# Kernel tuning notes

Hardware: AMD Instinct MI355X
Metric: run time of the kernel (lower is better)

## Reference

```python
import jax, jax.numpy as jnp
import numpy as np

DIM = 768
HEADS = 12
HEAD_DIM = DIM // HEADS
SCALE = HEAD_DIM ** -0.5
EPS = 1e-6


def setup_inputs() -> dict:
    key = jax.random.key(0)
    ks = jax.random.split(key, 10)
    B, Nq, Nk, C = 4, 4096, 4096, DIM
    std = C ** -0.5
    return {
        "x_q": jax.random.normal(ks[0], (B, Nq, C), jnp.float32),
        "x_kv": jax.random.normal(ks[1], (B, Nk, C), jnp.float32),
        "Wq": jax.random.normal(ks[2], (C, C), jnp.float32) * std,
        "bq": jnp.zeros((C,), jnp.float32),
        "Wk": jax.random.normal(ks[3], (C, C), jnp.float32) * std,
        "bk": jnp.zeros((C,), jnp.float32),
        "Wv": jax.random.normal(ks[4], (C, C), jnp.float32) * std,
        "bv": jnp.zeros((C,), jnp.float32),
        "Wp": jax.random.normal(ks[5], (C, C), jnp.float32) * std,
        "bp": jnp.zeros((C,), jnp.float32),
    }


def _phi(x):
    # ELU(alpha=1) + 1 positive feature map
    return jax.nn.elu(x) + 1.0


def reference(x_q, x_kv, Wq, bq, Wk, bk, Wv, bv, Wp, bp):
    B, Nq, C = x_q.shape
    Nk = x_kv.shape[1]
    h, d = HEADS, HEAD_DIM
    # projections (torch Linear: x @ W.T + b)
    q = x_q @ Wq.T + bq   # [B,Nq,C]
    k = x_kv @ Wk.T + bk  # [B,Nk,C]
    v = x_kv @ Wv.T + bv  # [B,Nk,C]
    # split heads -> [B,h,N,d]
    q = q.reshape(B, Nq, h, d).transpose(0, 2, 1, 3) * SCALE
    k = k.reshape(B, Nk, h, d).transpose(0, 2, 1, 3)
    v = v.reshape(B, Nk, h, d).transpose(0, 2, 1, 3)
    q_phi = _phi(q)
    k_phi = _phi(k)
    # KV state [B,h,d,d] and normalizer sum [B,h,d]
    kv = jnp.einsum('bhnd,bhne->bhde', k_phi, v)
    k_sum = k_phi.sum(axis=2)
    out = jnp.einsum('bhnd,bhde->bhne', q_phi, kv)
    z = jnp.einsum('bhnd,bhd->bhn', q_phi, k_sum)[..., None] + EPS
    out = out / z
    out = out.transpose(0, 2, 1, 3).reshape(B, Nq, C)
    return out @ Wp.T + bp
```

## Files before the change

### kernel.cpp

```cpp
#include <hip/hip_runtime.h>
#include <hip/hip_bf16.h>
#include <cstdint>
#include <cstddef>

#define HD_B   4
#define SEQ    4096
#define CDIM   768
#define HEADS  12
#define HDIM   64
#define MROWS  (HD_B * SEQ)
#define QSCALE 0.125f
#define EPSV   1e-6f

typedef __attribute__((ext_vector_type(8))) short  short8v;
typedef __attribute__((ext_vector_type(4))) float  f32x4;

__device__ __forceinline__ unsigned short f2b(float f) {
    unsigned int u = __float_as_uint(f);
    u += 0x7FFFu + ((u >> 16) & 1u);
    return (unsigned short)(u >> 16);
}
__device__ __forceinline__ float b2f(unsigned short b) {
    return __uint_as_float(((unsigned int)b) << 16);
}
__device__ __forceinline__ float phi_f(float x) {
    return x > 0.f ? x + 1.f : __expf(x);
}

#define GLOAD_LDS16(g, l)                                             \
    __builtin_amdgcn_global_load_lds(                                 \
        (__attribute__((address_space(1))) void*)(void*)(g),          \
        (__attribute__((address_space(3))) void*)(l), 16, 0, 0)

#define VMW12() asm volatile("s_waitcnt vmcnt(12)" ::: "memory")
#define VMW8()  asm volatile("s_waitcnt vmcnt(8)"  ::: "memory")
#define VMW4()  asm volatile("s_waitcnt vmcnt(4)"  ::: "memory")
#define VMW0()  asm volatile("s_waitcnt vmcnt(0)"  ::: "memory")
#define LGW()   asm volatile("s_waitcnt lgkmcnt(0)" ::: "memory")
#define SB()    do { __builtin_amdgcn_sched_barrier(0);               \
                     __builtin_amdgcn_s_barrier();                    \
                     __builtin_amdgcn_sched_barrier(0); } while (0)

__global__ void wcvt_all(const float* __restrict__ wq, const float* __restrict__ wk,
                         const float* __restrict__ wv, const float* __restrict__ wp,
                         unsigned short* __restrict__ dst) {
    const int y = blockIdx.y;
    const float* src = (y == 0) ? wq : (y == 1) ? wk : (y == 2) ? wv : wp;
    const int i = blockIdx.x * 256 + threadIdx.x;
    float4 v = reinterpret_cast<const float4*>(src)[i];
    ushort4 o;
    o.x = f2b(v.x); o.y = f2b(v.y); o.z = f2b(v.z); o.w = f2b(v.w);
    reinterpret_cast<ushort4*>(dst + (size_t)y * (CDIM * CDIM))[i] = o;
}

__global__ __launch_bounds__(256) void gemm_q(
    const float* __restrict__ A32,
    const unsigned short* __restrict__ Bp,
    const float* __restrict__ bias,
    unsigned short* __restrict__ outp)
{
    constexpr int K = CDIM;
    __shared__ __align__(16) char smem[32768];
    char* As = smem;
    char* Bs = smem + 16384;

    const int tid  = threadIdx.x;
    const int lane = tid & 63;
    const int w    = tid >> 6;
    const int wr   = w >> 1, wc = w & 1;
    const int brow = blockIdx.x * 128;
    const int bcol = blockIdx.y * 128;

    const int r8  = lane >> 3;
    const int c8e = ((lane & 7) ^ r8) << 3;
    const int ar  = lane >> 4;
    const int ac  = (lane & 15) << 2;
    const int fr  = lane & 15;
    const int hi4 = lane >> 4;

    f32x4 acc[4][4];
#pragma unroll
    for (int i = 0; i < 4; ++i)
#pragma unroll
        for (int j = 0; j < 4; ++j)
            acc[i][j] = (f32x4){0.f, 0.f, 0.f, 0.f};

    for (int k0 = 0; k0 < K; k0 += 64) {
#pragma unroll
        for (int g = 0; g < 4; ++g) {
            const unsigned short* src =
                Bp + (size_t)(bcol + w * 32 + g * 8 + r8) * K + k0 + c8e;
            GLOAD_LDS16(src, Bs + (w * 32 + g * 8) * 128);
        }
#pragma unroll
        for (int j = 0; j < 8; ++j) {
            const int row = w * 32 + j * 4 + ar;
            float4 f = *(const float4*)(A32 + (size_t)(brow + row) * K + k0 + ac);
            unsigned int p0, p1;
            asm("v_cvt_pk_bf16_f32 %0, %1, %2" : "=v"(p0) : "v"(f.x), "v"(f.y));
            asm("v_cvt_pk_bf16_f32 %0, %1, %2" : "=v"(p1) : "v"(f.z), "v"(f.w));
            uint2 pk; pk.x = p0; pk.y = p1;
            *(uint2*)(As + row * 128 + ((ac << 1) ^ ((row & 7) << 4))) = pk;
        }
        __syncthreads();

        short8v a[4][2], b[4][2];
#pragma unroll
        for (int i = 0; i < 4; ++i) {
            const int row = wr * 64 + i * 16 + fr;
#pragma unroll
            for (int ks = 0; ks < 2; ++ks)
                a[i][ks] = *(const short8v*)(As + row * 128 +
                              ((((ks << 2) + hi4) ^ (row & 7)) << 4));
        }
#pragma unroll
        for (int j = 0; j < 4; ++j) {
            const int row = wc * 64 + j * 16 + fr;
#pragma unroll
            for (int ks = 0; ks < 2; ++ks)
                b[j][ks] = *(const short8v*)(Bs + row * 128 +
                              ((((ks << 2) + hi4) ^ (row & 7)) << 4));
        }
#pragma unroll
        for (int i = 0; i < 4; ++i)
#pragma unroll
            for (int j = 0; j < 4; ++j) {
                acc[i][j] = __builtin_amdgcn_mfma_f32_16x16x32_bf16(a[i][0], b[j][0], acc[i][j], 0, 0, 0);
                acc[i][j] = __builtin_amdgcn_mfma_f32_16x16x32_bf16(a[i][1], b[j][1], acc[i][j], 0, 0, 0);
            }
        __syncthreads();
    }

    float* ep = (float*)(void*)smem + w * (16 * 68);
    const int rr = lane >> 2;
    const int cb = (lane & 3) * 4;
    float4 bb[4];
#pragma unroll
    for (int q = 0; q < 4; ++q)
        bb[q] = *(const float4*)&bias[bcol + wc * 64 + q * 16 + cb];
#pragma unroll
    for (int i = 0; i < 4; ++i) {
#pragma unroll
        for (int j = 0; j < 4; ++j)
#pragma unroll
            for (int r = 0; r < 4; ++r)
                ep[(hi4 * 4 + r) * 68 + j * 16 + fr] = acc[i][j][r];
#pragma unroll
        for (int q = 0; q < 4; ++q) {
            const int cc = q * 16 + cb;
            f32x4 v = *(const f32x4*)&ep[rr * 68 + cc];
            const int rg = brow + wr * 64 + i * 16 + rr;
            const int cg = bcol + wc * 64 + cc;
            const float4 bq = bb[q];
            ushort4 ov;
            ov.x = f2b(phi_f((v[0] + bq.x) * QSCALE));
            ov.y = f2b(phi_f((v[1] + bq.y) * QSCALE));
            ov.z = f2b(phi_f((v[2] + bq.z) * QSCALE));
            ov.w = f2b(phi_f((v[3] + bq.w) * QSCALE));
            *(ushort4*)(outp + (size_t)rg * 768 + cg) = ov;
        }
    }
}

template <int KIND>
__global__ __launch_bounds__(256, 3) void gemm_p2(
    const float* __restrict__ A32,
    const unsigned short* __restrict__ Abf,
    const unsigned short* __restrict__ Bp,
    const float* __restrict__ b0, const float* __restrict__ b1,
    unsigned short* __restrict__ out_k, unsigned short* __restrict__ out_v,
    float* __restrict__ out_f)
{
    constexpr int K  = CDIM;
    constexpr int NC = (KIND == 0) ? 12 : 6;
    constexpr int T  = NC * 128;
    constexpr int NT = K / 64;

    __shared__ __align__(16) char smem[49152];
    char* As = smem;

    const int tid  = threadIdx.x;
    const int lane = tid & 63;
    const int w    = tid >> 6;
    const int wr   = w >> 1, wc = w & 1;

    const int bid  = blockIdx.x;
    const int s    = (bid & 7) * (T >> 3) + (bid >> 3);
    const int colp = s % NC;
    const int rowp = s / NC;
    const int brow = rowp * 128;
    const int bcol = colp * 128;

    const int r8  = lane >> 3;
    const int c8e = ((lane & 7) ^ r8) << 3;
    const int ar  = lane >> 4;
    const int ac  = (lane & 15) << 2;
    const int fr  = lane & 15;
    const int hi4 = lane >> 4;

    f32x4 acc[4][4];
#pragma unroll
    for (int i = 0; i < 4; ++i)
#pragma unroll
        for (int j = 0; j < 4; ++j)
            acc[i][j] = (f32x4){0.f, 0.f, 0.f, 0.f};

    auto stageB = [&](int buf, int kt) {
        char* dst = smem + 16384 + buf * 16384;
#pragma unroll
        for (int g = 0; g < 4; ++g) {
            const unsigned short* src =
                Bp + (size_t)(bcol + w * 32 + g * 8 + r8) * K + kt * 64 + c8e;
            GLOAD_LDS16(src, dst + (w * 32 + g * 8) * 128);
        }
    };

    float4 fA[8];
    int4   rAb[4];
    auto aload = [&](int kt) {
        if (KIND == 0) {
#pragma unroll
            for (int j = 0; j < 8; ++j)
                fA[j] = *(const float4*)(A32 + (size_t)(brow + w * 32 + j * 4 + ar) * K
                                         + kt * 64 + ac);
        } else {
#pragma unroll
            for (int g = 0; g < 4; ++g)
                rAb[g] = *(const int4*)(Abf + (size_t)(brow + w * 32 + g * 8 + r8) * K
                                        + kt * 64 + ((lane & 7) << 3));
        }
    };
    auto awrite = [&]() {
        if (KIND == 0) {
#pragma unroll
            for (int j = 0; j < 8; ++j) {
                const int row = w * 32 + j * 4 + ar;
                unsigned int p0, p1;
                asm("v_cvt_pk_bf16_f32 %0, %1, %2" : "=v"(p0) : "v"(fA[j].x), "v"(fA[j].y));
                asm("v_cvt_pk_bf16_f32 %0, %1, %2" : "=v"(p1) : "v"(fA[j].z), "v"(fA[j].w));
                uint2 pk; pk.x = p0; pk.y = p1;
                *(uint2*)(As + row * 128 + ((ac << 1) ^ ((row & 7) << 4))) = pk;
            }
        } else {
#pragma unroll
            for (int g = 0; g < 4; ++g) {
                const int row = w * 32 + g * 8 + r8;
                *(int4*)(As + row * 128 + (((lane & 7) ^ r8) << 4)) = rAb[g];
            }
        }
    };
    auto compute = [&](int bbuf) {
        const char* Bb = smem + 16384 + bbuf * 16384;
        short8v a[4][2];
#pragma unroll
        for (int i = 0; i < 4; ++i) {
            const int row = wr * 64 + i * 16 + fr;
#pragma unroll
            for (int ks = 0; ks < 2; ++ks)
                a[i][ks] = *(const short8v*)(As + row * 128 +
                              ((((ks << 2) + hi4) ^ (row & 7)) << 4));
        }
#pragma unroll
        for (int j = 0; j < 4; ++j) {
            const int row = wc * 64 + j * 16 + fr;
            short8v bb0 = *(const short8v*)(Bb + row * 128 + ((hi4 ^ (row & 7)) << 4));
            short8v bb1 = *(const short8v*)(Bb + row * 128 + (((4 + hi4) ^ (row & 7)) << 4));
#pragma unroll
            for (int i = 0; i < 4; ++i) {
                acc[i][j] = __builtin_amdgcn_mfma_f32_16x16x32_bf16(a[i][0], bb0, acc[i][j], 0, 0, 0);
                acc[i][j] = __builtin_amdgcn_mfma_f32_16x16x32_bf16(a[i][1], bb1, acc[i][j], 0, 0, 0);
            }
        }
    };

    aload(0);
    stageB(0, 0);
    VMW4();
    awrite();
    aload(1);
    stageB(1, 1);
    LGW();
    SB();

    for (int t = 0; t < NT; ++t) {
        const int c = t & 1;
        if (t == NT - 1) { VMW0(); }
        else if (KIND == 0) { VMW12(); }
        else { VMW8(); }
        SB();
        compute(c);
        SB();
        if (t < NT - 1) {
            VMW4();
            awrite();
            if (t < NT - 2) { aload(t + 2); stageB(c, t + 2); }
            LGW();
        }
    }

    float* ep = (float*)(void*)smem + w * (16 * 68);
    const int rr = lane >> 2;
    const int cb = (lane & 3) * 4;
    const bool isV = (KIND == 0) && (colp >= 6);
    const float* bptr = (KIND == 1) ? b0 : (isV ? (b1 + (bcol - 768)) : (b0 + bcol));
    const int colbase = ((KIND == 0 && isV) ? bcol - 768 : bcol) + wc * 64;
    unsigned short* o16 = isV ? out_v : out_k;

    float4 bb[4];
#pragma unroll
    for (int q = 0; q < 4; ++q)
        bb[q] = (KIND == 1)
            ? *(const float4*)&bptr[bcol + wc * 64 + q * 16 + cb]
            : *(const float4*)&bptr[wc * 64 + q * 16 + cb];

#pragma unroll
    for (int i = 0; i < 4; ++i) {
#pragma unroll
        for (int j = 0; j < 4; ++j)
#pragma unroll
            for (int r = 0; r < 4; ++r)
                ep[(hi4 * 4 + r) * 68 + j * 16 + fr] = acc[i][j][r];
#pragma unroll
        for (int q = 0; q < 4; ++q) {
            const int cc = q * 16 + cb;
            f32x4 v = *(const f32x4*)&ep[rr * 68 + cc];
            const int rg = brow + wr * 64 + i * 16 + rr;
            const float4 bq = bb[q];
            if (KIND == 1) {
                float4 ov;
                ov.x = v[0] + bq.x; ov.y = v[1] + bq.y;
                ov.z = v[2] + bq.z; ov.w = v[3] + bq.w;
                *(float4*)(out_f + (size_t)rg * 768 + (bcol + wc * 64 + cc)) = ov;
            } else {
                ushort4 ov;
                if (!isV) {
                    ov.x = f2b(phi_f(v[0] + bq.x));
                    ov.y = f2b(phi_f(v[1] + bq.y));
                    ov.z = f2b(phi_f(v[2] + bq.z));
                    ov.w = f2b(phi_f(v[3] + bq.w));
                } else {
                    ov.x = f2b(v[0] + bq.x);
                    ov.y = f2b(v[1] + bq.y);
                    ov.z = f2b(v[2] + bq.z);
                    ov.w = f2b(v[3] + bq.w);
                }
                *(ushort4*)(o16 + (size_t)rg * 768 + (colbase + cc)) = ov;
            }
        }
    }
}

#define KVCH   128
#define KVITER 2
#define NCHUNK 16

__global__ __launch_bounds__(256) void kv_part(
    const unsigned short* __restrict__ kphi,
    const unsigned short* __restrict__ vmat,
    float* __restrict__ part)
{
    const int bh = blockIdx.y;
    const int b  = bh / HEADS, h = bh % HEADS;
    const int c  = blockIdx.x;
    __shared__ float Kl[KVCH][HDIM];
    __shared__ float Vl[KVCH][HDIM];
    const int t  = threadIdx.x;
    const int i  = t >> 2;
    const int jb = t & 3;

    float acc[16];
#pragma unroll
    for (int jj = 0; jj < 16; ++jj) acc[jj] = 0.f;
    float ksum = 0.f;

    for (int it = 0; it < KVITER; ++it) {
        const size_t rbase = (size_t)b * SEQ + (size_t)c * (KVCH * KVITER) + it * KVCH;
        __syncthreads();
        for (int l = 0; l < KVCH / 32; ++l) {
            int row = l * 32 + (t >> 3);
            int col = (t & 7) << 3;
            const size_t g = (rbase + row) * CDIM + h * HDIM + col;
            int4 kk = *(const int4*)(kphi + g);
            int4 vv = *(const int4*)(vmat + g);
            const unsigned short* kp = (const unsigned short*)&kk;
            const unsigned short* vp = (const unsigned short*)&vv;
#pragma unroll
            for (int q = 0; q < 8; ++q) {
                Kl[row][col + q] = b2f(kp[q]);
                Vl[row][col + q] = b2f(vp[q]);
            }
        }
        __syncthreads();
        for (int n = 0; n < KVCH; ++n) {
            float kf = Kl[n][i];
            const float4* vr = (const float4*)&Vl[n][jb * 16];
            float4 v0 = vr[0], v1 = vr[1], v2 = vr[2], v3 = vr[3];
            acc[0]  += kf * v0.x; acc[1]  += kf * v0.y; acc[2]  += kf * v0.z; acc[3]  += kf * v0.w;
            acc[4]  += kf * v1.x; acc[5]  += kf * v1.y; acc[6]  += kf * v1.z; acc[7]  += kf * v1.w;
            acc[8]  += kf * v2.x; acc[9]  += kf * v2.y; acc[10] += kf * v2.z; acc[11] += kf * v2.w;
            acc[12] += kf * v3.x; acc[13] += kf * v3.y; acc[14] += kf * v3.z; acc[15] += kf * v3.w;
            ksum += kf;
        }
    }
    float* op = part + ((size_t)c * 48 + bh) * 4160;
#pragma unroll
    for (int jj = 0; jj < 16; ++jj) op[i * 64 + jb * 16 + jj] = acc[jj];
    if (jb == 0) op[4096 + i] = ksum;
}

__global__ void kv_finalize(const float* __restrict__ part, float* __restrict__ kv) {
    int idx = blockIdx.x * 256 + threadIdx.x;
    if (idx >= 48 * 4160) return;
    float s = 0.f;
    for (int c = 0; c < NCHUNK; ++c) s += part[(size_t)c * 48 * 4160 + idx];
    kv[idx] = s;
}

__global__ __launch_bounds__(256) void attn_apply(
    const unsigned short* __restrict__ qphi,
    const float* __restrict__ kv,
    unsigned short* __restrict__ attn)
{
    const int h  = blockIdx.y;
    const int m0 = blockIdx.x * 64;
    const int b  = m0 >> 12;
    const int bh = b * HEADS + h;
    __shared__ float kvs[HDIM][HDIM];
    __shared__ float ksums[HDIM];
    __shared__ unsigned short ql[64][HDIM];
    const int t = threadIdx.x;
    const float* kvp = kv + (size_t)bh * 4160;
#pragma unroll
    for (int it = 0; it < 4; ++it) {
        int e = it * 1024 + t * 4;
        *(float4*)&kvs[e >> 6][e & 63] = *(const float4*)&kvp[e];
    }
    if (t < 64) ksums[t] = kvp[4096 + t];
#pragma unroll
    for (int it = 0; it < 2; ++it) {
        int row = it * 32 + (t >> 3);
        int col = (t & 7) << 3;
        *(int4*)&ql[row][col] =
            *(const int4*)(qphi + (size_t)(m0 + row) * CDIM + h * HDIM + col);
    }
    __syncthreads();

    const int r  = t >> 2;
    const int jb = t & 3;
    float acc[16];
#pragma unroll
    for (int jj = 0; jj < 16; ++jj) acc[jj] = 0.f;
    float z = 0.f;
    for (int q8 = 0; q8 < 8; ++q8) {
        short8v qv = *(const short8v*)&ql[r][q8 * 8];
#pragma unroll
        for (int dd = 0; dd < 8; ++dd) {
            float qd = b2f((unsigned short)qv[dd]);
            int d = q8 * 8 + dd;
            const float4* kr = (const float4*)&kvs[d][jb * 16];
            float4 k0 = kr[0], k1 = kr[1], k2 = kr[2], k3 = kr[3];
            acc[0]  += qd * k0.x; acc[1]  += qd * k0.y; acc[2]  += qd * k0.z; acc[3]  += qd * k0.w;
            acc[4]  += qd * k1.x; acc[5]  += qd * k1.y; acc[6]  += qd * k1.z; acc[7]  += qd * k1.w;
            acc[8]  += qd * k2.x; acc[9]  += qd * k2.y; acc[10] += qd * k2.z; acc[11] += qd * k2.w;
            acc[12] += qd * k3.x; acc[13] += qd * k3.y; acc[14] += qd * k3.z; acc[15] += qd * k3.w;
            z += qd * ksums[d];
        }
    }
    const float inv = 1.f / (z + EPSV);
    unsigned short* op = attn + (size_t)(m0 + r) * CDIM + h * HDIM + jb * 16;
#pragma unroll
    for (int jj = 0; jj < 16; ++jj) op[jj] = f2b(acc[jj] * inv);
}

extern "C" void kernel_launch(void* const* d_in, const int* in_sizes, int n_in,
                              void* d_out, int out_size, void* d_ws, size_t ws_size,
                              hipStream_t stream)
{
    const float* x_q  = (const float*)d_in[0];
    const float* x_kv = (const float*)d_in[1];
    const float* Wq   = (const float*)d_in[2];
    const float* bq   = (const float*)d_in[3];
    const float* Wk   = (const float*)d_in[4];
    const float* bk   = (const float*)d_in[5];
    const float* Wv   = (const float*)d_in[6];
    const float* bv   = (const float*)d_in[7];
    const float* Wp   = (const float*)d_in[8];
    const float* bp   = (const float*)d_in[9];
    float* out = (float*)d_out;

    char* ws = (char*)d_ws;
    size_t off = 0;
    auto alloc = [&](size_t bytes) -> char* {
        char* p = ws + off;
        off += (bytes + 255) & ~(size_t)255;
        return p;
    };
    const size_t xelems = (size_t)MROWS * CDIM;
    const size_t welems = (size_t)CDIM * CDIM;

    unsigned short* w16    = (unsigned short*)alloc(4 * welems * 2);
    unsigned short* wkv16  = w16 + welems;
    unsigned short* wp16   = w16 + 3 * welems;
    unsigned short* qphi   = (unsigned short*)alloc(xelems * 2);
    unsigned short* kphi   = (unsigned short*)alloc(xelems * 2);
    unsigned short* v16    = (unsigned short*)alloc(xelems * 2);
    unsigned short* attn16 = (unsigned short*)alloc(xelems * 2);
    float* part = (float*)alloc((size_t)NCHUNK * 48 * 4160 * 4);
    float* kvf  = (float*)alloc((size_t)48 * 4160 * 4);

    wcvt_all<<<dim3(576, 4), 256, 0, stream>>>(Wq, Wk, Wv, Wp, w16);

    gemm_q<<<dim3(128, 6), 256, 0, stream>>>(x_q, w16, bq, qphi);

    gemm_p2<0><<<1536, 256, 0, stream>>>(
        x_kv, nullptr, wkv16, bk, bv, kphi, v16, nullptr);

    kv_part<<<dim3(NCHUNK, 48), 256, 0, stream>>>(kphi, v16, part);
    kv_finalize<<<(48 * 4160 + 255) / 256, 256, 0, stream>>>(part, kvf);
    attn_apply<<<dim3(MROWS / 64, HEADS), 256, 0, stream>>>(qphi, kvf, attn16);

    gemm_p2<1><<<768, 256, 0, stream>>>(
        nullptr, attn16, wp16, bp, nullptr, nullptr, nullptr, out);
}
```

Before: 242.2 us.

## Swap Q and output GEMM kernels, add MFMA priority, shrink KV LDS

The Q projection now runs on the double-buffered, tile-swizzled pipelined GEMM body shared with the KV projection. The output projection moves to the simpler single-buffered kernel, which now loads both A and B directly to LDS. s_setprio is raised around the MFMA sections. kv_part keeps K in bf16 in LDS, uses vectorized V stores and requests 3 blocks per CU. Together these aim to improve overlap and occupancy, but the output GEMM may lose the pipelining it had before.

```diff
diff --git a/kernel.cpp b/kernel.cpp
--- a/kernel.cpp
+++ b/kernel.cpp
@@ -33,7 +33,6 @@
         (__attribute__((address_space(3))) void*)(l), 16, 0, 0)
 
 #define VMW12() asm volatile("s_waitcnt vmcnt(12)" ::: "memory")
-#define VMW8()  asm volatile("s_waitcnt vmcnt(8)"  ::: "memory")
 #define VMW4()  asm volatile("s_waitcnt vmcnt(4)"  ::: "memory")
 #define VMW0()  asm volatile("s_waitcnt vmcnt(0)"  ::: "memory")
 #define LGW()   asm volatile("s_waitcnt lgkmcnt(0)" ::: "memory")
@@ -53,23 +52,31 @@
     reinterpret_cast<ushort4*>(dst + (size_t)y * (CDIM * CDIM))[i] = o;
 }
 
-__global__ __launch_bounds__(256) void gemm_q(
+template <int EPI, int NC>
+__device__ __forceinline__ void proj_body(
     const float* __restrict__ A32,
     const unsigned short* __restrict__ Bp,
-    const float* __restrict__ bias,
-    unsigned short* __restrict__ outp)
-{
-    constexpr int K = CDIM;
-    __shared__ __align__(16) char smem[32768];
+    const float* __restrict__ b0, const float* __restrict__ b1,
+    unsigned short* __restrict__ o0, unsigned short* __restrict__ o1)
+{
+    constexpr int K  = CDIM;
+    constexpr int T  = NC * 128;
+    constexpr int NT = K / 64;
+
+    __shared__ __align__(16) char smem[49152];
     char* As = smem;
-    char* Bs = smem + 16384;
 
     const int tid  = threadIdx.x;
     const int lane = tid & 63;
     const int w    = tid >> 6;
     const int wr   = w >> 1, wc = w & 1;
-    const int brow = blockIdx.x * 128;
-    const int bcol = blockIdx.y * 128;
+
+    const int bid  = blockIdx.x;
+    const int s    = (bid & 7) * (T >> 3) + (bid >> 3);
+    const int colp = s % NC;
+    const int rowp = s / NC;
+    const int brow = rowp * 128;
+    const int bcol = colp * 128;
 
     const int r8  = lane >> 3;
     const int c8e = ((lane & 7) ^ r8) << 3;
@@ -85,126 +92,6 @@
         for (int j = 0; j < 4; ++j)
             acc[i][j] = (f32x4){0.f, 0.f, 0.f, 0.f};
 
-    for (int k0 = 0; k0 < K; k0 += 64) {
-#pragma unroll
-        for (int g = 0; g < 4; ++g) {
-            const unsigned short* src =
-                Bp + (size_t)(bcol + w * 32 + g * 8 + r8) * K + k0 + c8e;
-            GLOAD_LDS16(src, Bs + (w * 32 + g * 8) * 128);
-        }
-#pragma unroll
-        for (int j = 0; j < 8; ++j) {
-            const int row = w * 32 + j * 4 + ar;
-            float4 f = *(const float4*)(A32 + (size_t)(brow + row) * K + k0 + ac);
-            unsigned int p0, p1;
-            asm("v_cvt_pk_bf16_f32 %0, %1, %2" : "=v"(p0) : "v"(f.x), "v"(f.y));
-            asm("v_cvt_pk_bf16_f32 %0, %1, %2" : "=v"(p1) : "v"(f.z), "v"(f.w));
-            uint2 pk; pk.x = p0; pk.y = p1;
-            *(uint2*)(As + row * 128 + ((ac << 1) ^ ((row & 7) << 4))) = pk;
-        }
-        __syncthreads();
-
-        short8v a[4][2], b[4][2];
-#pragma unroll
-        for (int i = 0; i < 4; ++i) {
-            const int row = wr * 64 + i * 16 + fr;
-#pragma unroll
-            for (int ks = 0; ks < 2; ++ks)
-                a[i][ks] = *(const short8v*)(As + row * 128 +
-                              ((((ks << 2) + hi4) ^ (row & 7)) << 4));
-        }
-#pragma unroll
-        for (int j = 0; j < 4; ++j) {
-            const int row = wc * 64 + j * 16 + fr;
-#pragma unroll
-            for (int ks = 0; ks < 2; ++ks)
-                b[j][ks] = *(const short8v*)(Bs + row * 128 +
-                              ((((ks << 2) + hi4) ^ (row & 7)) << 4));
-        }
-#pragma unroll
-        for (int i = 0; i < 4; ++i)
-#pragma unroll
-            for (int j = 0; j < 4; ++j) {
-                acc[i][j] = __builtin_amdgcn_mfma_f32_16x16x32_bf16(a[i][0], b[j][0], acc[i][j], 0, 0, 0);
-                acc[i][j] = __builtin_amdgcn_mfma_f32_16x16x32_bf16(a[i][1], b[j][1], acc[i][j], 0, 0, 0);
-            }
-        __syncthreads();
-    }
-
-    float* ep = (float*)(void*)smem + w * (16 * 68);
-    const int rr = lane >> 2;
-    const int cb = (lane & 3) * 4;
-    float4 bb[4];
-#pragma unroll
-    for (int q = 0; q < 4; ++q)
-        bb[q] = *(const float4*)&bias[bcol + wc * 64 + q * 16 + cb];
-#pragma unroll
-    for (int i = 0; i < 4; ++i) {
-#pragma unroll
-        for (int j = 0; j < 4; ++j)
-#pragma unroll
-            for (int r = 0; r < 4; ++r)
-                ep[(hi4 * 4 + r) * 68 + j * 16 + fr] = acc[i][j][r];
-#pragma unroll
-        for (int q = 0; q < 4; ++q) {
-            const int cc = q * 16 + cb;
-            f32x4 v = *(const f32x4*)&ep[rr * 68 + cc];
-            const int rg = brow + wr * 64 + i * 16 + rr;
-            const int cg = bcol + wc * 64 + cc;
-            const float4 bq = bb[q];
-            ushort4 ov;
-            ov.x = f2b(phi_f((v[0] + bq.x) * QSCALE));
-            ov.y = f2b(phi_f((v[1] + bq.y) * QSCALE));
-            ov.z = f2b(phi_f((v[2] + bq.z) * QSCALE));
-            ov.w = f2b(phi_f((v[3] + bq.w) * QSCALE));
-            *(ushort4*)(outp + (size_t)rg * 768 + cg) = ov;
-        }
-    }
-}
-
-template <int KIND>
-__global__ __launch_bounds__(256, 3) void gemm_p2(
-    const float* __restrict__ A32,
-    const unsigned short* __restrict__ Abf,
-    const unsigned short* __restrict__ Bp,
-    const float* __restrict__ b0, const float* __restrict__ b1,
-    unsigned short* __restrict__ out_k, unsigned short* __restrict__ out_v,
-    float* __restrict__ out_f)
-{
-    constexpr int K  = CDIM;
-    constexpr int NC = (KIND == 0) ? 12 : 6;
-    constexpr int T  = NC * 128;
-    constexpr int NT = K / 64;
-
-    __shared__ __align__(16) char smem[49152];
-    char* As = smem;
-
-    const int tid  = threadIdx.x;
-    const int lane = tid & 63;
-    const int w    = tid >> 6;
-    const int wr   = w >> 1, wc = w & 1;
-
-    const int bid  = blockIdx.x;
-    const int s    = (bid & 7) * (T >> 3) + (bid >> 3);
-    const int colp = s % NC;
-    const int rowp = s / NC;
-    const int brow = rowp * 128;
-    const int bcol = colp * 128;
-
-    const int r8  = lane >> 3;
-    const int c8e = ((lane & 7) ^ r8) << 3;
-    const int ar  = lane >> 4;
-    const int ac  = (lane & 15) << 2;
-    const int fr  = lane & 15;
-    const int hi4 = lane >> 4;
-
-    f32x4 acc[4][4];
-#pragma unroll
-    for (int i = 0; i < 4; ++i)
-#pragma unroll
-        for (int j = 0; j < 4; ++j)
-            acc[i][j] = (f32x4){0.f, 0.f, 0.f, 0.f};
-
     auto stageB = [&](int buf, int kt) {
         char* dst = smem + 16384 + buf * 16384;
 #pragma unroll
@@ -216,37 +103,21 @@
     };
 
     float4 fA[8];
-    int4   rAb[4];
     auto aload = [&](int kt) {
-        if (KIND == 0) {
-#pragma unroll
-            for (int j = 0; j < 8; ++j)
-                fA[j] = *(const float4*)(A32 + (size_t)(brow + w * 32 + j * 4 + ar) * K
-                                         + kt * 64 + ac);
-        } else {
-#pragma unroll
-            for (int g = 0; g < 4; ++g)
-                rAb[g] = *(const int4*)(Abf + (size_t)(brow + w * 32 + g * 8 + r8) * K
-                                        + kt * 64 + ((lane & 7) << 3));
-        }
+#pragma unroll
+        for (int j = 0; j < 8; ++j)
+            fA[j] = *(const float4*)(A32 + (size_t)(brow + w * 32 + j * 4 + ar) * K
+                                     + kt * 64 + ac);
     };
     auto awrite = [&]() {
-        if (KIND == 0) {
-#pragma unroll
-            for (int j = 0; j < 8; ++j) {
-                const int row = w * 32 + j * 4 + ar;
-                unsigned int p0, p1;
-                asm("v_cvt_pk_bf16_f32 %0, %1, %2" : "=v"(p0) : "v"(fA[j].x), "v"(fA[j].y));
-                asm("v_cvt_pk_bf16_f32 %0, %1, %2" : "=v"(p1) : "v"(fA[j].z), "v"(fA[j].w));
-                uint2 pk; pk.x = p0; pk.y = p1;
-                *(uint2*)(As + row * 128 + ((ac << 1) ^ ((row & 7) << 4))) = pk;
-            }
-        } else {
-#pragma unroll
-            for (int g = 0; g < 4; ++g) {
-                const int row = w * 32 + g * 8 + r8;
-                *(int4*)(As + row * 128 + (((lane & 7) ^ r8) << 4)) = rAb[g];
-            }
+#pragma unroll
+        for (int j = 0; j < 8; ++j) {
+            const int row = w * 32 + j * 4 + ar;
+            unsigned int p0, p1;
+            asm("v_cvt_pk_bf16_f32 %0, %1, %2" : "=v"(p0) : "v"(fA[j].x), "v"(fA[j].y));
+            asm("v_cvt_pk_bf16_f32 %0, %1, %2" : "=v"(p1) : "v"(fA[j].z), "v"(fA[j].w));
+            uint2 pk; pk.x = p0; pk.y = p1;
+            *(uint2*)(As + row * 128 + ((ac << 1) ^ ((row & 7) << 4))) = pk;
         }
     };
     auto compute = [&](int bbuf) {
@@ -260,6 +131,7 @@
                 a[i][ks] = *(const short8v*)(As + row * 128 +
                               ((((ks << 2) + hi4) ^ (row & 7)) << 4));
         }
+        __builtin_amdgcn_s_setprio(1);
 #pragma unroll
         for (int j = 0; j < 4; ++j) {
             const int row = wc * 64 + j * 16 + fr;
@@ -271,6 +143,7 @@
                 acc[i][j] = __builtin_amdgcn_mfma_f32_16x16x32_bf16(a[i][1], bb1, acc[i][j], 0, 0, 0);
             }
         }
+        __builtin_amdgcn_s_setprio(0);
     };
 
     aload(0);
@@ -284,9 +157,7 @@
 
     for (int t = 0; t < NT; ++t) {
         const int c = t & 1;
-        if (t == NT - 1) { VMW0(); }
-        else if (KIND == 0) { VMW12(); }
-        else { VMW8(); }
+        if (t == NT - 1) { VMW0(); } else { VMW12(); }
         SB();
         compute(c);
         SB();
@@ -301,17 +172,16 @@
     float* ep = (float*)(void*)smem + w * (16 * 68);
     const int rr = lane >> 2;
     const int cb = (lane & 3) * 4;
-    const bool isV = (KIND == 0) && (colp >= 6);
-    const float* bptr = (KIND == 1) ? b0 : (isV ? (b1 + (bcol - 768)) : (b0 + bcol));
-    const int colbase = ((KIND == 0 && isV) ? bcol - 768 : bcol) + wc * 64;
-    unsigned short* o16 = isV ? out_v : out_k;
+    const bool isV = (EPI == 1) && (colp >= 6);
+    const float* bptr = (EPI == 0) ? (b0 + bcol)
+                        : (isV ? (b1 + (bcol - 768)) : (b0 + bcol));
+    const int colbase = ((EPI == 1 && isV) ? bcol - 768 : bcol) + wc * 64;
+    unsigned short* o16 = (EPI == 1 && isV) ? o1 : o0;
 
     float4 bb[4];
 #pragma unroll
     for (int q = 0; q < 4; ++q)
-        bb[q] = (KIND == 1)
-            ? *(const float4*)&bptr[bcol + wc * 64 + q * 16 + cb]
-            : *(const float4*)&bptr[wc * 64 + q * 16 + cb];
+        bb[q] = *(const float4*)&bptr[wc * 64 + q * 16 + cb];
 
 #pragma unroll
     for (int i = 0; i < 4; ++i) {
@@ -326,26 +196,139 @@
             f32x4 v = *(const f32x4*)&ep[rr * 68 + cc];
             const int rg = brow + wr * 64 + i * 16 + rr;
             const float4 bq = bb[q];
-            if (KIND == 1) {
-                float4 ov;
-                ov.x = v[0] + bq.x; ov.y = v[1] + bq.y;
-                ov.z = v[2] + bq.z; ov.w = v[3] + bq.w;
-                *(float4*)(out_f + (size_t)rg * 768 + (bcol + wc * 64 + cc)) = ov;
+            ushort4 ov;
+            if (EPI == 0) {
+                ov.x = f2b(phi_f((v[0] + bq.x) * QSCALE));
+                ov.y = f2b(phi_f((v[1] + bq.y) * QSCALE));
+                ov.z = f2b(phi_f((v[2] + bq.z) * QSCALE));
+                ov.w = f2b(phi_f((v[3] + bq.w) * QSCALE));
+            } else if (!isV) {
+                ov.x = f2b(phi_f(v[0] + bq.x));
+                ov.y = f2b(phi_f(v[1] + bq.y));
+                ov.z = f2b(phi_f(v[2] + bq.z));
+                ov.w = f2b(phi_f(v[3] + bq.w));
             } else {
-                ushort4 ov;
-                if (!isV) {
-                    ov.x = f2b(phi_f(v[0] + bq.x));
-                    ov.y = f2b(phi_f(v[1] + bq.y));
-                    ov.z = f2b(phi_f(v[2] + bq.z));
-                    ov.w = f2b(phi_f(v[3] + bq.w));
-                } else {
-                    ov.x = f2b(v[0] + bq.x);
-                    ov.y = f2b(v[1] + bq.y);
-                    ov.z = f2b(v[2] + bq.z);
-                    ov.w = f2b(v[3] + bq.w);
-                }
-                *(ushort4*)(o16 + (size_t)rg * 768 + (colbase + cc)) = ov;
+                ov.x = f2b(v[0] + bq.x);
+                ov.y = f2b(v[1] + bq.y);
+                ov.z = f2b(v[2] + bq.z);
+                ov.w = f2b(v[3] + bq.w);
             }
+            *(ushort4*)(o16 + (size_t)rg * 768 + (colbase + cc)) = ov;
+        }
+    }
+}
+
+__global__ __launch_bounds__(256, 3) void g_q(
+    const float* __restrict__ xq, const unsigned short* __restrict__ wq,
+    const float* __restrict__ bq, unsigned short* __restrict__ qphi)
+{
+    proj_body<0, 6>(xq, wq, bq, nullptr, qphi, nullptr);
+}
+
+__global__ __launch_bounds__(256, 3) void g_kv(
+    const float* __restrict__ xkv, const unsigned short* __restrict__ wkv,
+    const float* __restrict__ bk, const float* __restrict__ bv,
+    unsigned short* __restrict__ kphi, unsigned short* __restrict__ v16)
+{
+    proj_body<1, 12>(xkv, wkv, bk, bv, kphi, v16);
+}
+
+__global__ __launch_bounds__(256) void g_out(
+    const unsigned short* __restrict__ A16,
+    const unsigned short* __restrict__ Bp,
+    const float* __restrict__ bias,
+    float* __restrict__ outp)
+{
+    constexpr int K = CDIM;
+    __shared__ __align__(16) char smem[32768];
+    char* As = smem;
+    char* Bs = smem + 16384;
+
+    const int tid  = threadIdx.x;
+    const int lane = tid & 63;
+    const int w    = tid >> 6;
+    const int wr   = w >> 1, wc = w & 1;
+    const int brow = blockIdx.x * 128;
+    const int bcol = blockIdx.y * 128;
+
+    const int r8  = lane >> 3;
+    const int c8e = ((lane & 7) ^ r8) << 3;
+    const int fr  = lane & 15;
+    const int hi4 = lane >> 4;
+
+    f32x4 acc[4][4];
+#pragma unroll
+    for (int i = 0; i < 4; ++i)
+#pragma unroll
+        for (int j = 0; j < 4; ++j)
+            acc[i][j] = (f32x4){0.f, 0.f, 0.f, 0.f};
+
+    for (int k0 = 0; k0 < K; k0 += 64) {
+#pragma unroll
+        for (int g = 0; g < 4; ++g) {
+            const unsigned short* srcA =
+                A16 + (size_t)(brow + w * 32 + g * 8 + r8) * K + k0 + c8e;
+            GLOAD_LDS16(srcA, As + (w * 32 + g * 8) * 128);
+            const unsigned short* srcB =
+                Bp + (size_t)(bcol + w * 32 + g * 8 + r8) * K + k0 + c8e;
+            GLOAD_LDS16(srcB, Bs + (w * 32 + g * 8) * 128);
+        }
+        __syncthreads();
+
+        short8v a[4][2], b[4][2];
+#pragma unroll
+        for (int i = 0; i < 4; ++i) {
+            const int row = wr * 64 + i * 16 + fr;
+#pragma unroll
+            for (int ks = 0; ks < 2; ++ks)
+                a[i][ks] = *(const short8v*)(As + row * 128 +
+                              ((((ks << 2) + hi4) ^ (row & 7)) << 4));
+        }
+#pragma unroll
+        for (int j = 0; j < 4; ++j) {
+            const int row = wc * 64 + j * 16 + fr;
+#pragma unroll
+            for (int ks = 0; ks < 2; ++ks)
+                b[j][ks] = *(const short8v*)(Bs + row * 128 +
+                              ((((ks << 2) + hi4) ^ (row & 7)) << 4));
+        }
+        __builtin_amdgcn_s_setprio(1);
+#pragma unroll
+        for (int i = 0; i < 4; ++i)
+#pragma unroll
+            for (int j = 0; j < 4; ++j) {
+                acc[i][j] = __builtin_amdgcn_mfma_f32_16x16x32_bf16(a[i][0], b[j][0], acc[i][j], 0, 0, 0);
+                acc[i][j] = __builtin_amdgcn_mfma_f32_16x16x32_bf16(a[i][1], b[j][1], acc[i][j], 0, 0, 0);
+            }
+        __builtin_amdgcn_s_setprio(0);
+        __syncthreads();
+    }
+
+    float* ep = (float*)(void*)smem + w * (16 * 68);
+    const int rr = lane >> 2;
+    const int cb = (lane & 3) * 4;
+    float4 bb[4];
+#pragma unroll
+    for (int q = 0; q < 4; ++q)
+        bb[q] = *(const float4*)&bias[bcol + wc * 64 + q * 16 + cb];
+#pragma unroll
+    for (int i = 0; i < 4; ++i) {
+#pragma unroll
+        for (int j = 0; j < 4; ++j)
+#pragma unroll
+            for (int r = 0; r < 4; ++r)
+                ep[(hi4 * 4 + r) * 68 + j * 16 + fr] = acc[i][j][r];
+#pragma unroll
+        for (int q = 0; q < 4; ++q) {
+            const int cc = q * 16 + cb;
+            f32x4 v = *(const f32x4*)&ep[rr * 68 + cc];
+            const int rg = brow + wr * 64 + i * 16 + rr;
+            const int cg = bcol + wc * 64 + cc;
+            const float4 bq = bb[q];
+            float4 ov;
+            ov.x = v[0] + bq.x; ov.y = v[1] + bq.y;
+            ov.z = v[2] + bq.z; ov.w = v[3] + bq.w;
+            *(float4*)(outp + (size_t)rg * 768 + cg) = ov;
         }
     }
 }
@@ -354,7 +337,7 @@
 #define KVITER 2
 #define NCHUNK 16
 
-__global__ __launch_bounds__(256) void kv_part(
+__global__ __launch_bounds__(256, 3) void kv_part(
     const unsigned short* __restrict__ kphi,
     const unsigned short* __restrict__ vmat,
     float* __restrict__ part)
@@ -362,7 +345,7 @@
     const int bh = blockIdx.y;
     const int b  = bh / HEADS, h = bh % HEADS;
     const int c  = blockIdx.x;
-    __shared__ float Kl[KVCH][HDIM];
+    __shared__ unsigned short Kl[KVCH][HDIM];
     __shared__ float Vl[KVCH][HDIM];
     const int t  = threadIdx.x;
     const int i  = t >> 2;
@@ -382,17 +365,17 @@
             const size_t g = (rbase + row) * CDIM + h * HDIM + col;
             int4 kk = *(const int4*)(kphi + g);
             int4 vv = *(const int4*)(vmat + g);
-            const unsigned short* kp = (const unsigned short*)&kk;
+            *(int4*)&Kl[row][col] = kk;
             const unsigned short* vp = (const unsigned short*)&vv;
-#pragma unroll
-            for (int q = 0; q < 8; ++q) {
-                Kl[row][col + q] = b2f(kp[q]);
-                Vl[row][col + q] = b2f(vp[q]);
-            }
+            float4 lo, hi;
+            lo.x = b2f(vp[0]); lo.y = b2f(vp[1]); lo.z = b2f(vp[2]); lo.w = b2f(vp[3]);
+            hi.x = b2f(vp[4]); hi.y = b2f(vp[5]); hi.z = b2f(vp[6]); hi.w = b2f(vp[7]);
+            *(float4*)&Vl[row][col]     = lo;
+            *(float4*)&Vl[row][col + 4] = hi;
         }
         __syncthreads();
         for (int n = 0; n < KVCH; ++n) {
-            float kf = Kl[n][i];
+            float kf = b2f(Kl[n][i]);
             const float4* vr = (const float4*)&Vl[n][jb * 16];
             float4 v0 = vr[0], v1 = vr[1], v2 = vr[2], v3 = vr[3];
             acc[0]  += kf * v0.x; acc[1]  += kf * v0.y; acc[2]  += kf * v0.z; acc[3]  += kf * v0.w;
@@ -510,15 +493,13 @@
 
     wcvt_all<<<dim3(576, 4), 256, 0, stream>>>(Wq, Wk, Wv, Wp, w16);
 
-    gemm_q<<<dim3(128, 6), 256, 0, stream>>>(x_q, w16, bq, qphi);
-
-    gemm_p2<0><<<1536, 256, 0, stream>>>(
-        x_kv, nullptr, wkv16, bk, bv, kphi, v16, nullptr);
+    g_q<<<768, 256, 0, stream>>>(x_q, w16, bq, qphi);
+
+    g_kv<<<1536, 256, 0, stream>>>(x_kv, wkv16, bk, bv, kphi, v16);
 
     kv_part<<<dim3(NCHUNK, 48), 256, 0, stream>>>(kphi, v16, part);
     kv_finalize<<<(48 * 4160 + 255) / 256, 256, 0, stream>>>(part, kvf);
     attn_apply<<<dim3(MROWS / 64, HEADS), 256, 0, stream>>>(qphi, kvf, attn16);
 
-    gemm_p2<1><<<768, 256, 0, stream>>>(
-        nullptr, attn16, wp16, bp, nullptr, nullptr, nullptr, out);
-}
+    g_out<<<dim3(128, 6), 256, 0, stream>>>(attn16, wp16, bp, out);
+}
```

Measured after the change: 244.9 us. No clear change (+1.1%).
